# Kernel tuning notes

Hardware: AMD Instinct MI355X
Metric: run time of the kernel (lower is better)

The kernel has to match this reference:

```python
import jax, jax.numpy as jnp
import numpy as np

HEAD_SIZE = 64
EMB_SIZE = 1024
B, T = 8, 2048


def setup_inputs() -> dict:
    key = jax.random.key(0)
    k_x, k_q, k_k, k_v, k_m = jax.random.split(key, 5)
    X = jax.random.normal(k_x, (B, T, EMB_SIZE), dtype=jnp.float32)
    # nn.Linear(emb, head, bias=False) weights have shape (head, emb)
    s = EMB_SIZE ** -0.5
    Wq = jax.random.uniform(k_q, (HEAD_SIZE, EMB_SIZE), jnp.float32, -s, s)
    Wk = jax.random.uniform(k_k, (HEAD_SIZE, EMB_SIZE), jnp.float32, -s, s)
    Wv = jax.random.uniform(k_v, (HEAD_SIZE, EMB_SIZE), jnp.float32, -s, s)
    padding_mask = jax.random.randint(k_m, (B, T), 0, 2).astype(bool)
    # ensure no row is fully masked (would yield NaN softmax)
    padding_mask = padding_mask.at[:, 0].set(False)
    return {"X": X, "Wq": Wq, "Wk": Wk, "Wv": Wv, "padding_mask": padding_mask}


def reference(X, Wq, Wk, Wv, padding_mask):
    # X: (B,T,C); W*: (H,C); padding_mask: (B,T) bool, True = masked key
    C = X.shape[-1]
    Q = jnp.einsum('btc,hc->bth', X, Wq)
    K = jnp.einsum('btc,hc->bth', X, Wk)
    V = jnp.einsum('btc,hc->bth', X, Wv)
    # NOTE: source scales by emb_size**-0.5 (C), not head_size**-0.5
    wei = jnp.einsum('bth,bsh->bts', Q, K) * (C ** -0.5)  # (B,T,T)
    wei = jnp.where(padding_mask[:, None, :], -jnp.inf, wei)
    wei = jax.nn.softmax(wei, axis=-1)  # dropout disabled (eval mode)
    out = jnp.einsum('bts,bsh->bth', wei, V)  # (B,T,H)
    return out
```

## Files before the change

kernel.cpp:

```cpp
#include <hip/hip_runtime.h>
#include <hip/hip_bf16.h>
#include <math.h>


#define T_SEQ 2048
#define EMB 1024
#define HS 64
#define NB 8

typedef __attribute__((ext_vector_type(8))) short short8;
typedef __attribute__((ext_vector_type(4))) float f32x4;
typedef __attribute__((ext_vector_type(2))) unsigned int uint2_t;
typedef unsigned short ushort_t;

static __device__ inline ushort_t f2bf(float f) {
  union { float f; unsigned u; } v; v.f = f;
  unsigned r = v.u + 0x7FFF + ((v.u >> 16) & 1);
  return (ushort_t)(r >> 16);
}
static __device__ inline unsigned pk2(float a, float b) {
  return (unsigned)f2bf(a) | ((unsigned)f2bf(b) << 16);
}

__global__ __launch_bounds__(256) void convw_kernel(
    const float* __restrict__ Wq, const float* __restrict__ Wk,
    const float* __restrict__ Wv, ushort_t* __restrict__ Wb) {
  const int m = blockIdx.x >> 4;
  const int blk = blockIdx.x & 15;
  const float* src = (m == 0) ? Wq : (m == 1) ? Wk : Wv;
  const float scale = (m == 0) ? 0.03125f : 1.0f;
  const int base = blk * 4096 + threadIdx.x * 16;
  ushort_t* dst = Wb + m * 65536;
  ushort_t tmp[16];
#pragma unroll
  for (int j = 0; j < 4; ++j) {
    float4 x = *(const float4*)(src + base + j * 4);
    tmp[j * 4 + 0] = f2bf(x.x * scale);
    tmp[j * 4 + 1] = f2bf(x.y * scale);
    tmp[j * 4 + 2] = f2bf(x.z * scale);
    tmp[j * 4 + 3] = f2bf(x.w * scale);
  }
  *(short8*)(dst + base) = *(short8*)tmp;
  *(short8*)(dst + base + 8) = *(short8*)(tmp + 8);
}

__global__ __launch_bounds__(256) void proj_kernel(
    const float* __restrict__ X, const ushort_t* __restrict__ Wb,
    ushort_t* __restrict__ Qb, ushort_t* __restrict__ Kb,
    ushort_t* __restrict__ Vtb) {
  __shared__ __align__(16) ushort_t Xs[2][32 * 256];
  const int tid = threadIdx.x;
  const int lane = tid & 63, w = tid >> 6;
  const int l15 = lane & 15, hi = lane >> 4;
  const long rbase = (long)blockIdx.x * 32;

  const ushort_t* Wrow[3];
#pragma unroll
  for (int t = 0; t < 3; ++t) {
    const int ht = 3 * w + t, m = ht >> 2, hs = ht & 3;
    Wrow[t] = Wb + m * 65536 + (hs * 16 + l15) * 1024 + hi * 8;
  }

  short8 wfA[6], wfB[6], wfC[6], wfD[6];
  auto loadw = [&](short8 (&dst)[6], int s) {
#pragma unroll
    for (int t = 0; t < 3; ++t) {
      dst[2 * t + 0] = *(const short8*)(Wrow[t] + s * 64);
      dst[2 * t + 1] = *(const short8*)(Wrow[t] + s * 64 + 32);
    }
  };
  loadw(wfA, 0); loadw(wfB, 1); loadw(wfC, 2);

  float4 xr[8];
  auto stage_load = [&](int c) {
#pragma unroll
    for (int j = 0; j < 8; ++j) {
      const int f = j * 256 + tid;
      const int row = f >> 6, c4 = f & 63;
      xr[j] = *(const float4*)(X + (rbase + row) * EMB + c * 256 + c4 * 4);
    }
  };
  auto stage_write = [&](int buf) {
    ushort_t* Xd = Xs[buf];
#pragma unroll
    for (int j = 0; j < 8; ++j) {
      const int f = j * 256 + tid;
      const int row = f >> 6, c4 = f & 63;
      uint2_t pv;
      pv.x = pk2(xr[j].x, xr[j].y);
      pv.y = pk2(xr[j].z, xr[j].w);
      *(uint2_t*)((char*)(Xd + row * 256) + ((c4 * 8) ^ ((row & 7) << 4))) = pv;
    }
  };

  f32x4 acc[2][3];
#pragma unroll
  for (int rt = 0; rt < 2; ++rt)
#pragma unroll
    for (int t = 0; t < 3; ++t) acc[rt][t] = (f32x4){0.f, 0.f, 0.f, 0.f};

  const int swA = (l15 & 7) << 4;

  auto body = [&](int sg, int buf, short8 (&cur)[6], short8 (&pre)[6]) {
    if (sg + 3 < 16) loadw(pre, sg + 3);
    const char* XrowA = (const char*)(Xs[buf] + l15 * 256);
    const char* XrowB = (const char*)(Xs[buf] + (16 + l15) * 256);
    const int sb = (sg & 3) * 128;
    short8 a0 = *(const short8*)(XrowA + ((sb + hi * 16) ^ swA));
    short8 a1 = *(const short8*)(XrowA + ((sb + 64 + hi * 16) ^ swA));
    short8 b0 = *(const short8*)(XrowB + ((sb + hi * 16) ^ swA));
    short8 b1 = *(const short8*)(XrowB + ((sb + 64 + hi * 16) ^ swA));
#pragma unroll
    for (int t = 0; t < 3; ++t) {
      acc[0][t] = __builtin_amdgcn_mfma_f32_16x16x32_bf16(a0, cur[2 * t + 0], acc[0][t], 0, 0, 0);
      acc[0][t] = __builtin_amdgcn_mfma_f32_16x16x32_bf16(a1, cur[2 * t + 1], acc[0][t], 0, 0, 0);
      acc[1][t] = __builtin_amdgcn_mfma_f32_16x16x32_bf16(b0, cur[2 * t + 0], acc[1][t], 0, 0, 0);
      acc[1][t] = __builtin_amdgcn_mfma_f32_16x16x32_bf16(b1, cur[2 * t + 1], acc[1][t], 0, 0, 0);
    }
  };

  stage_load(0);
  stage_write(0);
  __syncthreads();

#pragma unroll
  for (int c = 0; c < 4; ++c) {
    if (c < 3) stage_load(c + 1);
    body(c * 4 + 0, c & 1, wfA, wfD);
    body(c * 4 + 1, c & 1, wfB, wfA);
    body(c * 4 + 2, c & 1, wfC, wfB);
    body(c * 4 + 3, c & 1, wfD, wfC);
    if (c < 3) {
      stage_write((c + 1) & 1);
      __syncthreads();
    }
  }

  const long bblk = rbase >> 11;
  const long tb0 = rbase & 2047;
  ushort_t* outs[2] = {Qb, Kb};
#pragma unroll
  for (int rt = 0; rt < 2; ++rt)
#pragma unroll
    for (int t = 0; t < 3; ++t) {
      const int ht = 3 * w + t, m = ht >> 2, hs = ht & 3;
      const int h = hs * 16 + l15;
      if (m < 2) {
#pragma unroll
        for (int r = 0; r < 4; ++r) {
          const long row = rbase + rt * 16 + 4 * hi + r;
          outs[m][row * 64 + h] = f2bf(acc[rt][t][r]);
        }
      } else {
        const long tloc = tb0 + rt * 16 + 4 * hi;
        uint2_t v;
        v.x = pk2(acc[rt][t][0], acc[rt][t][1]);
        v.y = pk2(acc[rt][t][2], acc[rt][t][3]);
        *(uint2_t*)(Vtb + bblk * (long)HS * T_SEQ + (long)h * T_SEQ + tloc) = v;
      }
    }
}

__global__ __launch_bounds__(256) void attn_kernel(
    const ushort_t* __restrict__ Qb, const ushort_t* __restrict__ Kb,
    const ushort_t* __restrict__ Vtb, const int* __restrict__ mask,
    float* __restrict__ out) {
  __shared__ __align__(16) char Lds[78080];

  const int tid = threadIdx.x;
  const int lane = tid & 63, w = tid >> 6;
  const int l15 = lane & 15, hi = lane >> 4;
  const int qs = w & 1, g = w >> 1;
  const int si = tid & 127;
  const int id = blockIdx.x;
  const int b = id & 7;
  const int q0 = (id >> 3) * 32;

  ushort_t* biasB = (ushort_t*)(Lds + 73728);
  float* alphaArr = (float*)(Lds + 77824);

  {
    const ushort_t nb = f2bf(-1e30f);
    const int* mp = mask + b * T_SEQ + tid * 8;
    int4 m0 = *(const int4*)(mp);
    int4 m1 = *(const int4*)(mp + 4);
    ushort_t t8[8];
    t8[0] = m0.x ? nb : 0; t8[1] = m0.y ? nb : 0;
    t8[2] = m0.z ? nb : 0; t8[3] = m0.w ? nb : 0;
    t8[4] = m1.x ? nb : 0; t8[5] = m1.y ? nb : 0;
    t8[6] = m1.z ? nb : 0; t8[7] = m1.w ? nb : 0;
    *(short8*)(biasB + tid * 8) = *(short8*)t8;
  }

  const ushort_t* Qrow = Qb + (long)(b * T_SEQ + q0 + qs * 16 + l15) * 64;
  const short8 qf0 = *(const short8*)(Qrow + hi * 8);
  const short8 qf1 = *(const short8*)(Qrow + 32 + hi * 8);

  const ushort_t* Kg = Kb + (long)b * T_SEQ * 64;
  const ushort_t* Vg = Vtb + (long)b * HS * T_SEQ;

  short8 kreg[4], vreg[4];
  auto stage_load = [&](int t) {
    const ushort_t* ktile = Kg + (g * 1024 + t * 64) * 64;
#pragma unroll
    for (int j = 0; j < 4; ++j)
      kreg[j] = *(const short8*)(ktile + j * 1024 + si * 8);
    const ushort_t* vtile =
        Vg + (long)(si >> 1) * T_SEQ + g * 1024 + t * 64 + (si & 1) * 32;
#pragma unroll
    for (int j = 0; j < 4; ++j)
      vreg[j] = *(const short8*)(vtile + j * 8);
  };
  auto stage_write = [&](int buf) {
    char* Kd = Lds + (g * 2 + buf) * 8192;
#pragma unroll
    for (int j = 0; j < 4; ++j) {
      const int row = j * 16 + (si >> 3);
      *(short8*)(Kd + row * 128 + (((si & 7) * 16) ^ ((row & 7) << 4))) = kreg[j];
    }
    char* Vd = Lds + 32768 + (g * 2 + buf) * 8192;
    const int vrow = si >> 1, sv = (vrow & 7) << 4;
#pragma unroll
    for (int j = 0; j < 4; ++j)
      *(short8*)(Vd + vrow * 128 + ((((si & 1) * 64) + j * 16) ^ sv)) = vreg[j];
  };

  f32x4 O[4];
#pragma unroll
  for (int ht = 0; ht < 4; ++ht) O[ht] = (f32x4){0.f, 0.f, 0.f, 0.f};
  float mrow = -1e30f, lsum = 0.f;

  char* prow = Lds + 65536 + w * 2048 + l15 * 128;
  const int sw = (l15 & 7) << 4;
  const int swr = (l15 & 7) << 4;

  stage_load(0);
  stage_write(0);
  __syncthreads();

#pragma unroll 1
  for (int t = 0; t < 16; ++t) {
    if (t < 15) stage_load(t + 1);
    const int buf = t & 1;

    f32x4 s[4];
    const char* Kl = Lds + (g * 2 + buf) * 8192;
    __builtin_amdgcn_s_setprio(1);
#pragma unroll
    for (int kt = 0; kt < 4; ++kt) {
      const char* kr = Kl + (kt * 16 + l15) * 128;
      short8 k0 = *(const short8*)(kr + ((hi * 16) ^ swr));
      short8 k1 = *(const short8*)(kr + ((64 + hi * 16) ^ swr));
      f32x4 z = {0.f, 0.f, 0.f, 0.f};
      s[kt] = __builtin_amdgcn_mfma_f32_16x16x32_bf16(k0, qf0, z, 0, 0, 0);
      s[kt] = __builtin_amdgcn_mfma_f32_16x16x32_bf16(k1, qf1, s[kt], 0, 0, 0);
    }
    __builtin_amdgcn_s_setprio(0);

    const ushort_t* blp = biasB + g * 1024 + t * 64;
#pragma unroll
    for (int kt = 0; kt < 4; ++kt) {
      const uint2_t bu = *(const uint2_t*)(blp + kt * 16 + hi * 4);
      union { unsigned u; float f; } c0, c1, c2, c3;
      c0.u = bu.x << 16; c1.u = bu.x & 0xFFFF0000u;
      c2.u = bu.y << 16; c3.u = bu.y & 0xFFFF0000u;
      s[kt][0] += c0.f; s[kt][1] += c1.f;
      s[kt][2] += c2.f; s[kt][3] += c3.f;
    }

    float t0m = fmaxf(fmaxf(s[0][0], s[0][1]), fmaxf(s[0][2], s[0][3]));
    float t1m = fmaxf(fmaxf(s[1][0], s[1][1]), fmaxf(s[1][2], s[1][3]));
    float t2m = fmaxf(fmaxf(s[2][0], s[2][1]), fmaxf(s[2][2], s[2][3]));
    float t3m = fmaxf(fmaxf(s[3][0], s[3][1]), fmaxf(s[3][2], s[3][3]));
    float mt = fmaxf(fmaxf(t0m, t1m), fmaxf(t2m, t3m));
    mt = fmaxf(mt, __shfl_xor(mt, 16, 64));
    mt = fmaxf(mt, __shfl_xor(mt, 32, 64));

    const bool skip = __all(mt <= mrow + 8.0f);
    float mnew = mrow;
    if (!skip) {
      mnew = fmaxf(mrow, mt);
      const float alpha = __expf(mrow - mnew);
      if (lane < 16) alphaArr[w * 16 + l15] = alpha;
      lsum *= alpha;
      mrow = mnew;
    }

    float psum = 0.f;
#pragma unroll
    for (int kt = 0; kt < 4; ++kt) {
      const float p0 = __expf(s[kt][0] - mnew);
      const float p1 = __expf(s[kt][1] - mnew);
      const float p2 = __expf(s[kt][2] - mnew);
      const float p3 = __expf(s[kt][3] - mnew);
      psum += (p0 + p1) + (p2 + p3);
      const int a0 = (kt * 32 + hi * 8) ^ sw;
      *(unsigned*)(prow + a0) = pk2(p0, p1);
      *(unsigned*)(prow + a0 + 4) = pk2(p2, p3);
    }
    lsum += psum;

    if (!skip) {
      const f32x4 av = *(const f32x4*)(alphaArr + w * 16 + 4 * hi);
#pragma unroll
      for (int ht = 0; ht < 4; ++ht) O[ht] *= av;
    }

    short8 pa0 = *(const short8*)(prow + ((hi * 16) ^ sw));
    short8 pa1 = *(const short8*)(prow + ((64 + hi * 16) ^ sw));
    const char* Vl = Lds + 32768 + (g * 2 + buf) * 8192;
    __builtin_amdgcn_s_setprio(1);
#pragma unroll
    for (int ht = 0; ht < 4; ++ht) {
      const char* vr = Vl + (ht * 16 + l15) * 128;
      short8 v0 = *(const short8*)(vr + ((hi * 16) ^ swr));
      short8 v1 = *(const short8*)(vr + ((64 + hi * 16) ^ swr));
      O[ht] = __builtin_amdgcn_mfma_f32_16x16x32_bf16(pa0, v0, O[ht], 0, 0, 0);
      O[ht] = __builtin_amdgcn_mfma_f32_16x16x32_bf16(pa1, v1, O[ht], 0, 0, 0);
    }
    __builtin_amdgcn_s_setprio(0);

    if (t < 15) stage_write((t + 1) & 1);
    __syncthreads();
  }

  lsum += __shfl_xor(lsum, 16, 64);
  lsum += __shfl_xor(lsum, 32, 64);

  float* mergeF = (float*)Lds;
  if (g == 1) {
    float* ml = mergeF + (qs * 64 + lane) * 18;
    ml[0] = mrow; ml[1] = lsum;
#pragma unroll
    for (int ht = 0; ht < 4; ++ht)
#pragma unroll
      for (int r = 0; r < 4; ++r) ml[2 + ht * 4 + r] = O[ht][r];
  }
  __syncthreads();
  if (g == 0) {
    const float* ml = mergeF + (qs * 64 + lane) * 18;
    const float mB = ml[0], lB = ml[1];
    const float mn = fmaxf(mrow, mB);
    const float aa = __expf(mrow - mn);
    const float ab = __expf(mB - mn);
    const float inv = 1.0f / (lsum * aa + lB * ab);
    float* ob = out + (long)(b * T_SEQ + q0 + qs * 16) * 64;
#pragma unroll
    for (int r = 0; r < 4; ++r) {
      const float aar = __shfl(aa, 4 * hi + r, 64);
      const float abr = __shfl(ab, 4 * hi + r, 64);
      const float invr = __shfl(inv, 4 * hi + r, 64);
#pragma unroll
      for (int ht = 0; ht < 4; ++ht)
        ob[(4 * hi + r) * 64 + ht * 16 + l15] =
            (O[ht][r] * aar + ml[2 + ht * 4 + r] * abr) * invr;
    }
  }
}

extern "C" void kernel_launch(void* const* d_in, const int* in_sizes, int n_in,
                              void* d_out, int out_size, void* d_ws, size_t ws_size,
                              hipStream_t stream) {
  const float* X  = (const float*)d_in[0];
  const float* Wq = (const float*)d_in[1];
  const float* Wk = (const float*)d_in[2];
  const float* Wv = (const float*)d_in[3];
  const int* mask = (const int*)d_in[4];
  float* outp = (float*)d_out;

  const long NT = (long)NB * T_SEQ * HS;
  ushort_t* wsb = (ushort_t*)d_ws;
  ushort_t* Qb  = wsb;
  ushort_t* Kb  = wsb + NT;
  ushort_t* Vtb = wsb + 2 * NT;
  ushort_t* Wb  = wsb + 3 * NT;

  convw_kernel<<<48, 256, 0, stream>>>(Wq, Wk, Wv, Wb);
  proj_kernel<<<(NB * T_SEQ) / 32, 256, 0, stream>>>(X, Wb, Qb, Kb, Vtb);
  attn_kernel<<<512, 256, 0, stream>>>(Qb, Kb, Vtb, mask, outp);
}
```

Measured before the change: 67.40 us.

## Stage X tiles directly into LDS as fp32 via global_load_lds, convert at use

The projection kernel now copies X tiles from global memory straight into shared memory as fp32 using async global_load_lds with a swizzled source address. This replaces the old register-staged load, bf16 pack and LDS write. The bf16 conversion moves into the MFMA inner loop, so each wave converts its own A fragments on every use. The goal is to drop the register round-trip and VGPR pressure of the staging path. The cost is a shared-memory tile twice as large, twice the LDS read bandwidth, repeated conversions, and a barrier added on the final iteration.

Measured after the change: 70.26 us. +4.2%, slower.

```diff
diff --git a/kernel.cpp b/kernel.cpp
--- a/kernel.cpp
+++ b/kernel.cpp
@@ -21,6 +21,11 @@
 static __device__ inline unsigned pk2(float a, float b) {
   return (unsigned)f2bf(a) | ((unsigned)f2bf(b) << 16);
 }
+
+#define GL16(g, l)                                                   \
+  __builtin_amdgcn_global_load_lds(                                  \
+      (const __attribute__((address_space(1))) void*)(g),            \
+      (__attribute__((address_space(3))) void*)(l), 16, 0, 0)
 
 __global__ __launch_bounds__(256) void convw_kernel(
     const float* __restrict__ Wq, const float* __restrict__ Wk,
@@ -48,7 +53,7 @@
     const float* __restrict__ X, const ushort_t* __restrict__ Wb,
     ushort_t* __restrict__ Qb, ushort_t* __restrict__ Kb,
     ushort_t* __restrict__ Vtb) {
-  __shared__ __align__(16) ushort_t Xs[2][32 * 256];
+  __shared__ __align__(16) float Xsf[2][32 * 256];
   const int tid = threadIdx.x;
   const int lane = tid & 63, w = tid >> 6;
   const int l15 = lane & 15, hi = lane >> 4;
@@ -71,25 +76,14 @@
   };
   loadw(wfA, 0); loadw(wfB, 1); loadw(wfC, 2);
 
-  float4 xr[8];
-  auto stage_load = [&](int c) {
+  auto stage_gl = [&](int c, int buf) {
+    char* lbase = (char*)Xsf[buf];
 #pragma unroll
     for (int j = 0; j < 8; ++j) {
-      const int f = j * 256 + tid;
-      const int row = f >> 6, c4 = f & 63;
-      xr[j] = *(const float4*)(X + (rbase + row) * EMB + c * 256 + c4 * 4);
-    }
-  };
-  auto stage_write = [&](int buf) {
-    ushort_t* Xd = Xs[buf];
-#pragma unroll
-    for (int j = 0; j < 8; ++j) {
-      const int f = j * 256 + tid;
-      const int row = f >> 6, c4 = f & 63;
-      uint2_t pv;
-      pv.x = pk2(xr[j].x, xr[j].y);
-      pv.y = pk2(xr[j].z, xr[j].w);
-      *(uint2_t*)((char*)(Xd + row * 256) + ((c4 * 8) ^ ((row & 7) << 4))) = pv;
+      const int F = j * 256 + tid;
+      const int row = F >> 6, sl = F & 63;
+      const int gsl = sl ^ (row & 7);
+      GL16(X + (rbase + row) * EMB + c * 256 + gsl * 4, lbase + F * 16);
     }
   };
 
@@ -100,40 +94,47 @@
     for (int t = 0; t < 3; ++t) acc[rt][t] = (f32x4){0.f, 0.f, 0.f, 0.f};
 
   const int swA = (l15 & 7) << 4;
+
+  auto mk = [&](float4 f0, float4 f1) -> short8 {
+    ushort_t t8[8] = {f2bf(f0.x), f2bf(f0.y), f2bf(f0.z), f2bf(f0.w),
+                      f2bf(f1.x), f2bf(f1.y), f2bf(f1.z), f2bf(f1.w)};
+    return *(short8*)t8;
+  };
 
   auto body = [&](int sg, int buf, short8 (&cur)[6], short8 (&pre)[6]) {
     if (sg + 3 < 16) loadw(pre, sg + 3);
-    const char* XrowA = (const char*)(Xs[buf] + l15 * 256);
-    const char* XrowB = (const char*)(Xs[buf] + (16 + l15) * 256);
-    const int sb = (sg & 3) * 128;
-    short8 a0 = *(const short8*)(XrowA + ((sb + hi * 16) ^ swA));
-    short8 a1 = *(const short8*)(XrowA + ((sb + 64 + hi * 16) ^ swA));
-    short8 b0 = *(const short8*)(XrowB + ((sb + hi * 16) ^ swA));
-    short8 b1 = *(const short8*)(XrowB + ((sb + 64 + hi * 16) ^ swA));
-#pragma unroll
-    for (int t = 0; t < 3; ++t) {
-      acc[0][t] = __builtin_amdgcn_mfma_f32_16x16x32_bf16(a0, cur[2 * t + 0], acc[0][t], 0, 0, 0);
-      acc[0][t] = __builtin_amdgcn_mfma_f32_16x16x32_bf16(a1, cur[2 * t + 1], acc[0][t], 0, 0, 0);
-      acc[1][t] = __builtin_amdgcn_mfma_f32_16x16x32_bf16(b0, cur[2 * t + 0], acc[1][t], 0, 0, 0);
-      acc[1][t] = __builtin_amdgcn_mfma_f32_16x16x32_bf16(b1, cur[2 * t + 1], acc[1][t], 0, 0, 0);
-    }
-  };
-
-  stage_load(0);
-  stage_write(0);
+    const int bb = (sg & 3) * 256;
+#pragma unroll
+    for (int rt = 0; rt < 2; ++rt) {
+      const char* rowp = (const char*)(Xsf[buf] + (rt * 16 + l15) * 256);
+      const int b0 = bb + hi * 32;
+      float4 f0 = *(const float4*)(rowp + ((b0) ^ swA));
+      float4 f1 = *(const float4*)(rowp + ((b0 + 16) ^ swA));
+      float4 f2 = *(const float4*)(rowp + ((b0 + 128) ^ swA));
+      float4 f3 = *(const float4*)(rowp + ((b0 + 144) ^ swA));
+      short8 a0 = mk(f0, f1);
+      short8 a1 = mk(f2, f3);
+#pragma unroll
+      for (int t = 0; t < 3; ++t) {
+        acc[rt][t] = __builtin_amdgcn_mfma_f32_16x16x32_bf16(
+            a0, cur[2 * t + 0], acc[rt][t], 0, 0, 0);
+        acc[rt][t] = __builtin_amdgcn_mfma_f32_16x16x32_bf16(
+            a1, cur[2 * t + 1], acc[rt][t], 0, 0, 0);
+      }
+    }
+  };
+
+  stage_gl(0, 0);
   __syncthreads();
 
 #pragma unroll
   for (int c = 0; c < 4; ++c) {
-    if (c < 3) stage_load(c + 1);
+    if (c < 3) stage_gl(c + 1, (c + 1) & 1);
     body(c * 4 + 0, c & 1, wfA, wfD);
     body(c * 4 + 1, c & 1, wfB, wfA);
     body(c * 4 + 2, c & 1, wfC, wfB);
     body(c * 4 + 3, c & 1, wfD, wfC);
-    if (c < 3) {
-      stage_write((c + 1) & 1);
-      __syncthreads();
-    }
+    __syncthreads();
   }
 
   const long bblk = rbase >> 11;
```

## Double projection row tile to 64 rows with narrower 128-column X chunks

Applied to the files above, without the earlier changes.

The projection kernel now handles 64 rows of X per block instead of 32, with each staged X chunk narrowed from 256 to 128 columns so shared memory stays the same size. Every weight fragment loaded from global memory now feeds four row tiles instead of two, halving weight traffic per output row, and the grid shrinks to 256 blocks. The cost is more accumulator registers, twice as many chunk iterations and barriers, and fewer blocks to spread across the CUs.

New measurement: 59.16 us. 1.14x faster.

```diff
diff --git a/kernel.cpp b/kernel.cpp
--- a/kernel.cpp
+++ b/kernel.cpp
@@ -48,11 +48,11 @@
     const float* __restrict__ X, const ushort_t* __restrict__ Wb,
     ushort_t* __restrict__ Qb, ushort_t* __restrict__ Kb,
     ushort_t* __restrict__ Vtb) {
-  __shared__ __align__(16) ushort_t Xs[2][32 * 256];
+  __shared__ __align__(16) ushort_t Xs[2][64 * 128];
   const int tid = threadIdx.x;
   const int lane = tid & 63, w = tid >> 6;
   const int l15 = lane & 15, hi = lane >> 4;
-  const long rbase = (long)blockIdx.x * 32;
+  const long rbase = (long)blockIdx.x * 64;
 
   const ushort_t* Wrow[3];
 #pragma unroll
@@ -75,72 +75,77 @@
   auto stage_load = [&](int c) {
 #pragma unroll
     for (int j = 0; j < 8; ++j) {
-      const int f = j * 256 + tid;
-      const int row = f >> 6, c4 = f & 63;
-      xr[j] = *(const float4*)(X + (rbase + row) * EMB + c * 256 + c4 * 4);
+      const int F = j * 256 + tid;
+      const int row = F >> 5, c4 = F & 31;
+      xr[j] = *(const float4*)(X + (rbase + row) * EMB + c * 128 + c4 * 4);
     }
   };
   auto stage_write = [&](int buf) {
     ushort_t* Xd = Xs[buf];
 #pragma unroll
     for (int j = 0; j < 8; ++j) {
-      const int f = j * 256 + tid;
-      const int row = f >> 6, c4 = f & 63;
+      const int F = j * 256 + tid;
+      const int row = F >> 5, c4 = F & 31;
       uint2_t pv;
       pv.x = pk2(xr[j].x, xr[j].y);
       pv.y = pk2(xr[j].z, xr[j].w);
-      *(uint2_t*)((char*)(Xd + row * 256) + ((c4 * 8) ^ ((row & 7) << 4))) = pv;
-    }
-  };
-
-  f32x4 acc[2][3];
-#pragma unroll
-  for (int rt = 0; rt < 2; ++rt)
+      *(uint2_t*)((char*)(Xd + row * 128) + ((c4 * 8) ^ ((row & 7) << 4))) = pv;
+    }
+  };
+
+  f32x4 acc[4][3];
+#pragma unroll
+  for (int rt = 0; rt < 4; ++rt)
 #pragma unroll
     for (int t = 0; t < 3; ++t) acc[rt][t] = (f32x4){0.f, 0.f, 0.f, 0.f};
 
   const int swA = (l15 & 7) << 4;
 
-  auto body = [&](int sg, int buf, short8 (&cur)[6], short8 (&pre)[6]) {
-    if (sg + 3 < 16) loadw(pre, sg + 3);
-    const char* XrowA = (const char*)(Xs[buf] + l15 * 256);
-    const char* XrowB = (const char*)(Xs[buf] + (16 + l15) * 256);
-    const int sb = (sg & 3) * 128;
-    short8 a0 = *(const short8*)(XrowA + ((sb + hi * 16) ^ swA));
-    short8 a1 = *(const short8*)(XrowA + ((sb + 64 + hi * 16) ^ swA));
-    short8 b0 = *(const short8*)(XrowB + ((sb + hi * 16) ^ swA));
-    short8 b1 = *(const short8*)(XrowB + ((sb + 64 + hi * 16) ^ swA));
-#pragma unroll
-    for (int t = 0; t < 3; ++t) {
-      acc[0][t] = __builtin_amdgcn_mfma_f32_16x16x32_bf16(a0, cur[2 * t + 0], acc[0][t], 0, 0, 0);
-      acc[0][t] = __builtin_amdgcn_mfma_f32_16x16x32_bf16(a1, cur[2 * t + 1], acc[0][t], 0, 0, 0);
-      acc[1][t] = __builtin_amdgcn_mfma_f32_16x16x32_bf16(b0, cur[2 * t + 0], acc[1][t], 0, 0, 0);
-      acc[1][t] = __builtin_amdgcn_mfma_f32_16x16x32_bf16(b1, cur[2 * t + 1], acc[1][t], 0, 0, 0);
-    }
+  auto body = [&](int s, int buf, short8 (&cur)[6], short8 (&pre)[6]) {
+    if (s + 3 < 16) loadw(pre, s + 3);
+    const int sb = (s & 1) * 128;
+#pragma unroll
+    for (int rt = 0; rt < 4; ++rt) {
+      const char* rowp = (const char*)(Xs[buf] + (rt * 16 + l15) * 128);
+      short8 a0 = *(const short8*)(rowp + ((sb + hi * 16) ^ swA));
+      short8 a1 = *(const short8*)(rowp + ((sb + 64 + hi * 16) ^ swA));
+#pragma unroll
+      for (int t = 0; t < 3; ++t) {
+        acc[rt][t] = __builtin_amdgcn_mfma_f32_16x16x32_bf16(
+            a0, cur[2 * t + 0], acc[rt][t], 0, 0, 0);
+        acc[rt][t] = __builtin_amdgcn_mfma_f32_16x16x32_bf16(
+            a1, cur[2 * t + 1], acc[rt][t], 0, 0, 0);
+      }
+    }
+  };
+
+  auto chunk = [&](int c, short8 (&c0)[6], short8 (&p0)[6],
+                   short8 (&c1)[6], short8 (&p1)[6]) {
+    if (c < 7) stage_load(c + 1);
+    body(2 * c + 0, c & 1, c0, p0);
+    body(2 * c + 1, c & 1, c1, p1);
+    if (c < 7) stage_write((c + 1) & 1);
+    __syncthreads();
   };
 
   stage_load(0);
   stage_write(0);
   __syncthreads();
 
-#pragma unroll
-  for (int c = 0; c < 4; ++c) {
-    if (c < 3) stage_load(c + 1);
-    body(c * 4 + 0, c & 1, wfA, wfD);
-    body(c * 4 + 1, c & 1, wfB, wfA);
-    body(c * 4 + 2, c & 1, wfC, wfB);
-    body(c * 4 + 3, c & 1, wfD, wfC);
-    if (c < 3) {
-      stage_write((c + 1) & 1);
-      __syncthreads();
-    }
-  }
+  chunk(0, wfA, wfD, wfB, wfA);
+  chunk(1, wfC, wfB, wfD, wfC);
+  chunk(2, wfA, wfD, wfB, wfA);
+  chunk(3, wfC, wfB, wfD, wfC);
+  chunk(4, wfA, wfD, wfB, wfA);
+  chunk(5, wfC, wfB, wfD, wfC);
+  chunk(6, wfA, wfD, wfB, wfA);
+  chunk(7, wfC, wfB, wfD, wfC);
 
   const long bblk = rbase >> 11;
   const long tb0 = rbase & 2047;
   ushort_t* outs[2] = {Qb, Kb};
 #pragma unroll
-  for (int rt = 0; rt < 2; ++rt)
+  for (int rt = 0; rt < 4; ++rt)
 #pragma unroll
     for (int t = 0; t < 3; ++t) {
       const int ht = 3 * w + t, m = ht >> 2, hs = ht & 3;
@@ -376,6 +381,6 @@
   ushort_t* Wb  = wsb + 3 * NT;
 
   convw_kernel<<<48, 256, 0, stream>>>(Wq, Wk, Wv, Wb);
-  proj_kernel<<<(NB * T_SEQ) / 32, 256, 0, stream>>>(X, Wb, Qb, Kb, Vtb);
+  proj_kernel<<<(NB * T_SEQ) / 64, 256, 0, stream>>>(X, Wb, Qb, Kb, Vtb);
   attn_kernel<<<512, 256, 0, stream>>>(Qb, Kb, Vtb, mask, outp);
 }
```
